# Optimization experiments

Hardware: AMD Instinct MI355X
Metric: run time of the kernel (lower is better)

## Reference

```python
import jax, jax.numpy as jnp
import numpy as np

B, S, D = 1, 2048, 4096          # batch, seqlen, model dim
H, KVH, HD = 32, 8, 128          # query heads, kv heads, head dim
W = 1024                         # sliding window
ROPE_THETA = 10000.0


def _rope(t, cos, sin):
    # t: [b, s, h, hd]; complex pairing matches torch.view_as_complex on reshape(..., hd//2, 2)
    a = t[..., 0::2]
    b = t[..., 1::2]
    out_r = a * cos - b * sin
    out_i = a * sin + b * cos
    return jnp.stack([out_r, out_i], axis=-1).reshape(t.shape)


def setup_inputs() -> dict:
    key = jax.random.key(0)
    ks = jax.random.split(key, 5)
    x = jax.random.normal(ks[0], (1, B, S, D), dtype=jnp.float32)
    wq = jax.random.normal(ks[1], (H * HD, D), dtype=jnp.float32) * 0.02
    wk = jax.random.normal(ks[2], (KVH * HD, D), dtype=jnp.float32) * 0.02
    wv = jax.random.normal(ks[3], (KVH * HD, D), dtype=jnp.float32) * 0.02
    wo = jax.random.normal(ks[4], (D, H * HD), dtype=jnp.float32) * 0.02
    # rotary frequencies: freqs_cis[s, hd/2] = exp(i * s * theta^{-2k/hd})
    inv_freq = 1.0 / (ROPE_THETA ** (jnp.arange(0, HD, 2, dtype=jnp.float32) / HD))
    angles = jnp.arange(S, dtype=jnp.float32)[:, None] * inv_freq[None, :]  # [S, HD/2]
    freqs_cos = jnp.cos(angles)
    freqs_sin = jnp.sin(angles)
    # sliding-window causal mask (additive)
    i = jnp.arange(S)
    allowed = (i[:, None] >= i[None, :]) & (i[:, None] - i[None, :] < W)
    mask = jnp.where(allowed, 0.0, -1e9).astype(jnp.float32)
    positions = jnp.arange(S, dtype=jnp.int64)
    return {"x": x, "wq": wq, "wk": wk, "wv": wv, "wo": wo,
            "freqs_cos": freqs_cos, "freqs_sin": freqs_sin,
            "mask": mask, "positions": positions}


def reference(x, wq, wk, wv, wo, freqs_cos, freqs_sin, mask, positions):
    xs = x[0]                                   # [B, S, D]
    xq = (xs @ wq.T).reshape(B, S, H, HD)
    xk = (xs @ wk.T).reshape(B, S, KVH, HD)
    xv = (xs @ wv.T).reshape(B, S, KVH, HD)
    cos = freqs_cos[None, :, None, :]           # [1, S, 1, HD/2]
    sin = freqs_sin[None, :, None, :]
    xq = _rope(xq, cos, sin)
    xk = _rope(xk, cos, sin)
    # GQA: repeat_interleave kv heads to match query heads (prefill path)
    rep = H // KVH
    k = jnp.repeat(xk, rep, axis=2)             # [B, S, H, HD]
    v = jnp.repeat(xv, rep, axis=2)
    scale = HD ** -0.5
    scores = jnp.einsum('bqhd,bkhd->bhqk', xq, k) * scale + mask[None, None]
    probs = jax.nn.softmax(scores, axis=-1)
    out = jnp.einsum('bhqk,bkhd->bqhd', probs, v).reshape(B, S, H * HD)
    return (out @ wo.T)[None]                   # [1, B, S, D]
```

## Files before the change

### kernel.cpp

```cpp
#include <hip/hip_runtime.h>
#include <hip/hip_bf16.h>


typedef __attribute__((ext_vector_type(8))) short short8;
typedef __attribute__((ext_vector_type(4))) float floatx4;
typedef unsigned short u16;
typedef unsigned int u32;

__device__ __forceinline__ u16 f2bf(float f) {
  u32 u = __builtin_bit_cast(u32, f);
  u32 r = u + 0x7FFFu + ((u >> 16) & 1u);
  return (u16)(r >> 16);
}

#define GLDS16(g, l)                                                     \
  __builtin_amdgcn_global_load_lds(                                      \
      (const __attribute__((address_space(1))) u32*)(g),                 \
      (__attribute__((address_space(3))) u32*)(l), 16, 0, 0)

#define SB() __builtin_amdgcn_sched_barrier(0)

__global__ __launch_bounds__(256) void cast_all(
    const float* __restrict__ x, const float* __restrict__ wq,
    const float* __restrict__ wk, const float* __restrict__ wv,
    const float* __restrict__ wo, u16* __restrict__ xb, u16* __restrict__ wqb,
    u16* __restrict__ wkb, u16* __restrict__ wvb, u16* __restrict__ wob) {
  const int tid = blockIdx.x * blockDim.x + threadIdx.x;
  const int stride = gridDim.x * blockDim.x;
  auto seg = [&](const float* __restrict__ in, u16* __restrict__ out, int n4) {
    for (int i = tid; i < n4; i += stride) {
      float4 v = ((const float4*)in)[i];
      ushort4 o;
      o.x = f2bf(v.x); o.y = f2bf(v.y); o.z = f2bf(v.z); o.w = f2bf(v.w);
      ((ushort4*)out)[i] = o;
    }
  };
  seg(x, xb, 2097152);
  seg(wq, wqb, 4194304);
  seg(wk, wkb, 1048576);
  seg(wv, wvb, 1048576);
  seg(wo, wob, 4194304);
}

template <int IS_QKV>
__global__ __launch_bounds__(512, 2) void gemm_t(
    const u16* __restrict__ A, const u16* __restrict__ B, void* __restrict__ Cq,
    u16* __restrict__ Ck, u16* __restrict__ Cv, const float* __restrict__ fcos,
    const float* __restrict__ fsin) {
  constexpr int BM = IS_QKV ? 256 : 128;
  constexpr int BN = IS_QKV ? 192 : 256;
  constexpr int MFR = BM / 32;
  constexpr int NFR = BN / 64;
  constexpr int WC = BN / 4;
  constexpr int ASZ = BM * 128;
  constexpr int BSZ = BN * 128;
  constexpr int NCA = ASZ / 8192;
  constexpr int NCB = BSZ / 8192;
  __shared__ u16 lds[(2 * ASZ + 3 * BSZ) / 2];
  const int K = 4096;

  int bm, bx;
  if constexpr (IS_QKV) {
    bm = blockIdx.x & 7;
    bx = blockIdx.x >> 3;
  } else {
    const int xcd = blockIdx.x & 7;
    const int j = blockIdx.x >> 3;
    bm = xcd * 2 + (j & 1);
    bx = j >> 1;
  }
  const int m0 = bm * BM, n0 = bx * BN;

  const int t = threadIdx.x, l = t & 63, w = t >> 6;
  const int li = l & 15, g = l >> 4;
  const int wm = w >> 2, wn = w & 3;

  const int srow = t >> 3;
  const int sslot = (t & 7) ^ (srow & 7);
  const u16* gA = A + (size_t)(m0 + srow) * K + sslot * 8;
  const u16* gB = B + (size_t)(n0 + srow) * K + sslot * 8;
  const int dst = t * 16;

  char* A0p = (char*)lds;
  char* A1p = A0p + ASZ;
  char* B0p = A0p + 2 * ASZ;
  char* B1p = B0p + BSZ;
  char* B2p = B1p + BSZ;

  auto stA = [&](char* base, int kt, int c) {
    GLDS16(gA + (size_t)c * 64 * K + kt, base + c * 8192 + dst);
  };
  auto stB = [&](char* base, int kt, int c) {
    GLDS16(gB + (size_t)c * 64 * K + kt, base + c * 8192 + dst);
  };

  int offA[2][MFR], offB[2][NFR];
#pragma unroll
  for (int kh = 0; kh < 2; kh++) {
#pragma unroll
    for (int mf = 0; mf < MFR; mf++) {
      int r = wm * (BM / 2) + mf * 16 + li;
      offA[kh][mf] = r * 128 + ((((kh << 2) | g) ^ (r & 7)) << 4);
    }
#pragma unroll
    for (int nf = 0; nf < NFR; nf++) {
      int r = wn * WC + nf * 16 + li;
      offB[kh][nf] = r * 128 + ((((kh << 2) | g) ^ (r & 7)) << 4);
    }
  }

  floatx4 acc[MFR][NFR] = {};
  const int NT = K / 64;

#pragma unroll
  for (int c = 0; c < NCB; c++) stB(B0p, 0, c);
#pragma unroll
  for (int c = 0; c < NCA; c++) stA(A0p, 0, c);
#pragma unroll
  for (int c = 0; c < NCB; c++) stB(B1p, 64, c);
  if constexpr (IS_QKV) asm volatile("s_waitcnt vmcnt(3)" ::: "memory");
  else                  asm volatile("s_waitcnt vmcnt(4)" ::: "memory");
  __builtin_amdgcn_s_barrier();

  for (int tt = 0; tt < NT; ++tt) {
    const char* Ac = A0p;
    const char* Bc = B0p;
    const int kt1 = (tt + 1) * 64, kt2 = (tt + 2) * 64;
    const bool s1 = (tt + 1 < NT), s2 = (tt + 2 < NT);

    if constexpr (IS_QKV) {
      short8 afr[4], bfr[NFR];
#pragma unroll
      for (int nf = 0; nf < NFR; nf++) bfr[nf] = *(const short8*)(Bc + offB[0][nf]);
#pragma unroll
      for (int mf = 0; mf < 4; mf++) afr[mf] = *(const short8*)(Ac + offA[0][mf]);
      if (s1) { stA(A1p, kt1, 0); stA(A1p, kt1, 1); }
      SB(); __builtin_amdgcn_s_barrier();
      asm volatile("s_waitcnt lgkmcnt(0)" ::: "memory");
      SB(); __builtin_amdgcn_s_setprio(1);
#pragma unroll
      for (int mf = 0; mf < 4; mf++)
#pragma unroll
        for (int nf = 0; nf < NFR; nf++)
          acc[mf][nf] = __builtin_amdgcn_mfma_f32_16x16x32_bf16(afr[mf], bfr[nf], acc[mf][nf], 0, 0, 0);
      __builtin_amdgcn_s_setprio(0); SB(); __builtin_amdgcn_s_barrier();
#pragma unroll
      for (int mf = 0; mf < 4; mf++) afr[mf] = *(const short8*)(Ac + offA[0][4 + mf]);
      if (s1) { stA(A1p, kt1, 2); stA(A1p, kt1, 3); }
      SB(); __builtin_amdgcn_s_barrier();
      asm volatile("s_waitcnt lgkmcnt(0)" ::: "memory");
      SB(); __builtin_amdgcn_s_setprio(1);
#pragma unroll
      for (int mf = 0; mf < 4; mf++)
#pragma unroll
        for (int nf = 0; nf < NFR; nf++)
          acc[4 + mf][nf] = __builtin_amdgcn_mfma_f32_16x16x32_bf16(afr[mf], bfr[nf], acc[4 + mf][nf], 0, 0, 0);
      __builtin_amdgcn_s_setprio(0); SB(); __builtin_amdgcn_s_barrier();
#pragma unroll
      for (int nf = 0; nf < NFR; nf++) bfr[nf] = *(const short8*)(Bc + offB[1][nf]);
#pragma unroll
      for (int mf = 0; mf < 4; mf++) afr[mf] = *(const short8*)(Ac + offA[1][mf]);
      if (s2) { stB(B2p, kt2, 0); stB(B2p, kt2, 1); }
      SB(); __builtin_amdgcn_s_barrier();
      asm volatile("s_waitcnt lgkmcnt(0)" ::: "memory");
      SB(); __builtin_amdgcn_s_setprio(1);
#pragma unroll
      for (int mf = 0; mf < 4; mf++)
#pragma unroll
        for (int nf = 0; nf < NFR; nf++)
          acc[mf][nf] = __builtin_amdgcn_mfma_f32_16x16x32_bf16(afr[mf], bfr[nf], acc[mf][nf], 0, 0, 0);
      __builtin_amdgcn_s_setprio(0); SB(); __builtin_amdgcn_s_barrier();
#pragma unroll
      for (int mf = 0; mf < 4; mf++) afr[mf] = *(const short8*)(Ac + offA[1][4 + mf]);
      if (s2) stB(B2p, kt2, 2);
      SB(); __builtin_amdgcn_s_barrier();
      asm volatile("s_waitcnt lgkmcnt(0)" ::: "memory");
      SB(); __builtin_amdgcn_s_setprio(1);
#pragma unroll
      for (int mf = 0; mf < 4; mf++)
#pragma unroll
        for (int nf = 0; nf < NFR; nf++)
          acc[4 + mf][nf] = __builtin_amdgcn_mfma_f32_16x16x32_bf16(afr[mf], bfr[nf], acc[4 + mf][nf], 0, 0, 0);
      __builtin_amdgcn_s_setprio(0);
      if (s2) asm volatile("s_waitcnt vmcnt(3)" ::: "memory");
      else    asm volatile("s_waitcnt vmcnt(0)" ::: "memory");
      SB(); __builtin_amdgcn_s_barrier();
    } else {
      short8 afr[4], bfr[2];
#pragma unroll
      for (int mf = 0; mf < 4; mf++) afr[mf] = *(const short8*)(Ac + offA[0][mf]);
#pragma unroll
      for (int nf = 0; nf < 2; nf++) bfr[nf] = *(const short8*)(Bc + offB[0][nf]);
      if (s1) { stA(A1p, kt1, 0); stA(A1p, kt1, 1); }
      SB(); __builtin_amdgcn_s_barrier();
      asm volatile("s_waitcnt lgkmcnt(0)" ::: "memory");
      SB(); __builtin_amdgcn_s_setprio(1);
#pragma unroll
      for (int mf = 0; mf < 4; mf++)
#pragma unroll
        for (int nf = 0; nf < 2; nf++)
          acc[mf][nf] = __builtin_amdgcn_mfma_f32_16x16x32_bf16(afr[mf], bfr[nf], acc[mf][nf], 0, 0, 0);
      __builtin_amdgcn_s_setprio(0); SB(); __builtin_amdgcn_s_barrier();
#pragma unroll
      for (int nf = 0; nf < 2; nf++) bfr[nf] = *(const short8*)(Bc + offB[0][2 + nf]);
      if (s2) { stB(B2p, kt2, 0); stB(B2p, kt2, 1); }
      SB(); __builtin_amdgcn_s_barrier();
      asm volatile("s_waitcnt lgkmcnt(0)" ::: "memory");
      SB(); __builtin_amdgcn_s_setprio(1);
#pragma unroll
      for (int mf = 0; mf < 4; mf++)
#pragma unroll
        for (int nf = 0; nf < 2; nf++)
          acc[mf][2 + nf] = __builtin_amdgcn_mfma_f32_16x16x32_bf16(afr[mf], bfr[nf], acc[mf][2 + nf], 0, 0, 0);
      __builtin_amdgcn_s_setprio(0); SB(); __builtin_amdgcn_s_barrier();
#pragma unroll
      for (int mf = 0; mf < 4; mf++) afr[mf] = *(const short8*)(Ac + offA[1][mf]);
#pragma unroll
      for (int nf = 0; nf < 2; nf++) bfr[nf] = *(const short8*)(Bc + offB[1][nf]);
      if (s2) stB(B2p, kt2, 2);
      SB(); __builtin_amdgcn_s_barrier();
      asm volatile("s_waitcnt lgkmcnt(0)" ::: "memory");
      SB(); __builtin_amdgcn_s_setprio(1);
#pragma unroll
      for (int mf = 0; mf < 4; mf++)
#pragma unroll
        for (int nf = 0; nf < 2; nf++)
          acc[mf][nf] = __builtin_amdgcn_mfma_f32_16x16x32_bf16(afr[mf], bfr[nf], acc[mf][nf], 0, 0, 0);
      __builtin_amdgcn_s_setprio(0); SB(); __builtin_amdgcn_s_barrier();
#pragma unroll
      for (int nf = 0; nf < 2; nf++) bfr[nf] = *(const short8*)(Bc + offB[1][2 + nf]);
      if (s2) stB(B2p, kt2, 3);
      SB(); __builtin_amdgcn_s_barrier();
      asm volatile("s_waitcnt lgkmcnt(0)" ::: "memory");
      SB(); __builtin_amdgcn_s_setprio(1);
#pragma unroll
      for (int mf = 0; mf < 4; mf++)
#pragma unroll
        for (int nf = 0; nf < 2; nf++)
          acc[mf][2 + nf] = __builtin_amdgcn_mfma_f32_16x16x32_bf16(afr[mf], bfr[nf], acc[mf][2 + nf], 0, 0, 0);
      __builtin_amdgcn_s_setprio(0);
      if (s2) asm volatile("s_waitcnt vmcnt(4)" ::: "memory");
      else    asm volatile("s_waitcnt vmcnt(0)" ::: "memory");
      SB(); __builtin_amdgcn_s_barrier();
    }

    char* tmpA = A0p; A0p = A1p; A1p = tmpA;
    char* tmpB = B0p; B0p = B1p; B1p = B2p; B2p = tmpB;
  }

  const float scale = 0.08838834764831845f;
#pragma unroll
  for (int mf = 0; mf < MFR; mf++) {
#pragma unroll
    for (int nf = 0; nf < NFR; nf++) {
      const int row0 = m0 + wm * (BM / 2) + mf * 16 + 4 * g;
      const int c = n0 + wn * WC + nf * 16 + li;
      if constexpr (!IS_QKV) {
        float* Cf = (float*)Cq;
#pragma unroll
        for (int r = 0; r < 4; r++) Cf[(size_t)(row0 + r) * 4096 + c] = acc[mf][nf][r];
      } else {
        if (c < 5120) {
          const int hd = c & 127;
          const int pp = hd >> 1;
          const bool even = (hd & 1) == 0;
#pragma unroll
          for (int r = 0; r < 4; r++) {
            const int row = row0 + r;
            float cv = fcos[row * 64 + pp];
            float sv = fsin[row * 64 + pp];
            float v = acc[mf][nf][r];
            float pv = __shfl_xor(v, 1);
            float o = even ? (v * cv - pv * sv) : (pv * sv + v * cv);
            if (c < 4096) {
              ((u16*)Cq)[(size_t)row * 4096 + c] = f2bf(o * scale);
            } else {
              Ck[(size_t)row * 1024 + (c - 4096)] = f2bf(o);
            }
          }
        } else {
          u32 lo = (u32)f2bf(acc[mf][nf][0]) | ((u32)f2bf(acc[mf][nf][1]) << 16);
          u32 hi = (u32)f2bf(acc[mf][nf][2]) | ((u32)f2bf(acc[mf][nf][3]) << 16);
          uint2 val; val.x = lo; val.y = hi;
          *(uint2*)(&Cv[(size_t)(c - 5120) * 2048 + row0]) = val;
        }
      }
    }
  }
}

__global__ __launch_bounds__(256) void attn_kernel(const u16* __restrict__ Q,
                                                   const u16* __restrict__ K,
                                                   const u16* __restrict__ Vt,
                                                   u16* __restrict__ O) {
  __shared__ u16 Ks[2][64 * 128];
  __shared__ u16 Vs[2][128 * 64];
  __shared__ u16 Ps[4][16 * 72];

  const int t = threadIdx.x, l = t & 63, w = t >> 6;
  const int li = l & 15, g = l >> 4;
  const int q0 = blockIdx.x * 64;
  const int h = blockIdx.y;
  const int kvh = h >> 2;
  const int qw = q0 + w * 16;

  short8 qf[4];
  {
    const u16* qp = Q + (size_t)(qw + li) * 4096 + h * 128 + g * 8;
#pragma unroll
    for (int kk = 0; kk < 4; kk++) qf[kk] = *(const short8*)(qp + kk * 32);
  }

  const u16* gK[4];
  const u16* gV[4];
  int ldsOff[4];
#pragma unroll
  for (int i = 0; i < 4; i++) {
    int rK = 16 * w + 4 * i + (l >> 4);
    int sK = (l & 15) ^ (rK & 7);
    gK[i] = K + (size_t)rK * 1024 + kvh * 128 + sK * 8;
    int rV = 32 * w + 8 * i + (l >> 3);
    int sV = (l & 7) ^ (rV & 7);
    gV[i] = Vt + (size_t)(kvh * 128 + rV) * 2048 + sV * 8;
    ldsOff[i] = (4 * w + i) * 1024;
  }

  int offK[4][4];
#pragma unroll
  for (int n = 0; n < 4; n++) {
    int r = 16 * n + li;
#pragma unroll
    for (int kk = 0; kk < 4; kk++)
      offK[n][kk] = r * 256 + (((kk * 4 + g) ^ (r & 7)) << 4);
  }
  int offV[2][8];
#pragma unroll
  for (int kb = 0; kb < 2; kb++)
#pragma unroll
    for (int dt = 0; dt < 8; dt++) {
      int d = dt * 16 + li;
      offV[kb][dt] = d * 128 + (((kb * 4 + g) ^ (d & 7)) << 4);
    }

  float mrow[4] = {-1e30f, -1e30f, -1e30f, -1e30f};
  float lsum[4] = {0.f, 0.f, 0.f, 0.f};
  floatx4 accO[8] = {};

  int klo = q0 - 1023;
  if (klo < 0) klo = 0;
  klo &= ~63;
  const int nt = (q0 + 64 - klo) >> 6;

  auto stage = [&](int buf, int k0) {
    char* ksb = (char*)&Ks[buf][0];
    char* vsb = (char*)&Vs[buf][0];
#pragma unroll
    for (int i = 0; i < 4; i++) GLDS16(gK[i] + (size_t)k0 * 1024, ksb + ldsOff[i]);
#pragma unroll
    for (int i = 0; i < 4; i++) GLDS16(gV[i] + k0, vsb + ldsOff[i]);
  };

  stage(0, klo);
  asm volatile("s_waitcnt vmcnt(0)" ::: "memory");
  __builtin_amdgcn_s_barrier();

  for (int it = 0; it < nt; it++) {
    const int k0 = klo + (it << 6);
    if (it + 1 < nt) stage((it + 1) & 1, k0 + 64);

    if (k0 <= qw + 15 && k0 + 63 >= qw - 1023) {
      const char* kb = (const char*)&Ks[it & 1][0];
      const char* vb = (const char*)&Vs[it & 1][0];
      floatx4 s[4] = {};
      __builtin_amdgcn_s_setprio(1);
#pragma unroll
      for (int kk = 0; kk < 4; kk++)
#pragma unroll
        for (int n = 0; n < 4; n++) {
          short8 kf = *(const short8*)(kb + offK[n][kk]);
          s[n] = __builtin_amdgcn_mfma_f32_16x16x32_bf16(qf[kk], kf, s[n], 0, 0, 0);
        }
      __builtin_amdgcn_s_setprio(0);
      const bool full = (k0 + 63 <= qw) && (k0 >= qw + 15 - 1023);
      if (!full) {
#pragma unroll
        for (int n = 0; n < 4; n++) {
          const int kc = k0 + n * 16 + li;
#pragma unroll
          for (int r = 0; r < 4; r++) {
            const int qr = qw + 4 * g + r;
            if (kc > qr || qr - kc > 1023) s[n][r] = -__builtin_inff();
          }
        }
      }
      float rm[4];
#pragma unroll
      for (int r = 0; r < 4; r++)
        rm[r] = fmaxf(fmaxf(s[0][r], s[1][r]), fmaxf(s[2][r], s[3][r]));
#pragma unroll
      for (int msk = 1; msk <= 8; msk <<= 1)
#pragma unroll
        for (int r = 0; r < 4; r++) rm[r] = fmaxf(rm[r], __shfl_xor(rm[r], msk));
      float al[4];
#pragma unroll
      for (int r = 0; r < 4; r++) {
        float mn = fmaxf(mrow[r], rm[r]);
        al[r] = __expf(mrow[r] - mn);
        mrow[r] = mn;
        lsum[r] *= al[r];
      }
#pragma unroll
      for (int dt = 0; dt < 8; dt++)
#pragma unroll
        for (int r = 0; r < 4; r++) accO[dt][r] *= al[r];
      float rs[4] = {0.f, 0.f, 0.f, 0.f};
      u16* pw = &Ps[w][0];
#pragma unroll
      for (int n = 0; n < 4; n++)
#pragma unroll
        for (int r = 0; r < 4; r++) {
          float p = __expf(s[n][r] - mrow[r]);
          rs[r] += p;
          pw[(4 * g + r) * 72 + n * 16 + li] = f2bf(p);
        }
#pragma unroll
      for (int msk = 1; msk <= 8; msk <<= 1)
#pragma unroll
        for (int r = 0; r < 4; r++) rs[r] += __shfl_xor(rs[r], msk);
#pragma unroll
      for (int r = 0; r < 4; r++) lsum[r] += rs[r];
      short8 pa[2];
#pragma unroll
      for (int kbi = 0; kbi < 2; kbi++)
        pa[kbi] = *(const short8*)((const char*)&Ps[w][0] + li * 144 + kbi * 64 + g * 16);
      __builtin_amdgcn_s_setprio(1);
#pragma unroll
      for (int kbi = 0; kbi < 2; kbi++)
#pragma unroll
        for (int dt = 0; dt < 8; dt++) {
          short8 vf = *(const short8*)(vb + offV[kbi][dt]);
          accO[dt] = __builtin_amdgcn_mfma_f32_16x16x32_bf16(pa[kbi], vf, accO[dt], 0, 0, 0);
        }
      __builtin_amdgcn_s_setprio(0);
    }
    asm volatile("s_waitcnt vmcnt(0)" ::: "memory");
    __builtin_amdgcn_s_barrier();
  }

  float inv[4];
#pragma unroll
  for (int r = 0; r < 4; r++) inv[r] = 1.0f / lsum[r];
#pragma unroll
  for (int dt = 0; dt < 8; dt++)
#pragma unroll
    for (int r = 0; r < 4; r++)
      O[(size_t)(qw + 4 * g + r) * 4096 + h * 128 + dt * 16 + li] =
          f2bf(accO[dt][r] * inv[r]);
}

extern "C" void kernel_launch(void* const* d_in, const int* in_sizes, int n_in,
                              void* d_out, int out_size, void* d_ws, size_t ws_size,
                              hipStream_t stream) {
  const float* x    = (const float*)d_in[0];
  const float* wq   = (const float*)d_in[1];
  const float* wk   = (const float*)d_in[2];
  const float* wv   = (const float*)d_in[3];
  const float* wo   = (const float*)d_in[4];
  const float* fcos = (const float*)d_in[5];
  const float* fsin = (const float*)d_in[6];

  u16* ws  = (u16*)d_ws;
  u16* xb  = ws;
  u16* wqb = xb + 8388608;
  u16* wkb = wqb + 16777216;
  u16* wvb = wkb + 4194304;
  u16* wob = wvb + 4194304;
  u16* Qb  = wob + 16777216;
  u16* Kb  = Qb + 8388608;
  u16* Vtb = Kb + 2097152;
  u16* AOb = Vtb + 2097152;

  cast_all<<<2048, 256, 0, stream>>>(x, wq, wk, wv, wo, xb, wqb, wkb, wvb, wob);
  gemm_t<1><<<256, 512, 0, stream>>>(xb, wqb, Qb, Kb, Vtb, fcos, fsin);
  attn_kernel<<<dim3(32, 32), 256, 0, stream>>>(Qb, Kb, Vtb, AOb);
  gemm_t<0><<<256, 512, 0, stream>>>(AOb, wob, d_out, nullptr, nullptr, nullptr, nullptr);
}
```

Baseline: 321.0 us.

## Collapse GEMM K-loop into two phases and drop intra-iteration barriers

Restructures the main GEMM loop for both QKV and output projections into two half-K phases per 64-wide tile. Each phase loads full A/B fragments for that phase, then issues all MFMAs, with a single barrier at the end of the iteration instead of a barrier, lgkmcnt wait and setprio around every quarter. The goal is to cut synchronization overhead and let the compiler interleave LDS reads with MFMAs. In exchange it raises register pressure from the larger fragment arrays and drops the explicit wave priority and LDS-wait scheduling. It also relies on the compiler to insert correct LDS waits.

```diff
diff --git a/kernel.cpp b/kernel.cpp
--- a/kernel.cpp
+++ b/kernel.cpp
@@ -123,125 +123,64 @@
   __builtin_amdgcn_s_barrier();
 
   for (int tt = 0; tt < NT; ++tt) {
+    SB();
     const char* Ac = A0p;
     const char* Bc = B0p;
     const int kt1 = (tt + 1) * 64, kt2 = (tt + 2) * 64;
     const bool s1 = (tt + 1 < NT), s2 = (tt + 2 < NT);
 
     if constexpr (IS_QKV) {
-      short8 afr[4], bfr[NFR];
-#pragma unroll
-      for (int nf = 0; nf < NFR; nf++) bfr[nf] = *(const short8*)(Bc + offB[0][nf]);
-#pragma unroll
-      for (int mf = 0; mf < 4; mf++) afr[mf] = *(const short8*)(Ac + offA[0][mf]);
-      if (s1) { stA(A1p, kt1, 0); stA(A1p, kt1, 1); }
-      SB(); __builtin_amdgcn_s_barrier();
-      asm volatile("s_waitcnt lgkmcnt(0)" ::: "memory");
-      SB(); __builtin_amdgcn_s_setprio(1);
-#pragma unroll
-      for (int mf = 0; mf < 4; mf++)
-#pragma unroll
-        for (int nf = 0; nf < NFR; nf++)
-          acc[mf][nf] = __builtin_amdgcn_mfma_f32_16x16x32_bf16(afr[mf], bfr[nf], acc[mf][nf], 0, 0, 0);
-      __builtin_amdgcn_s_setprio(0); SB(); __builtin_amdgcn_s_barrier();
-#pragma unroll
-      for (int mf = 0; mf < 4; mf++) afr[mf] = *(const short8*)(Ac + offA[0][4 + mf]);
-      if (s1) { stA(A1p, kt1, 2); stA(A1p, kt1, 3); }
-      SB(); __builtin_amdgcn_s_barrier();
-      asm volatile("s_waitcnt lgkmcnt(0)" ::: "memory");
-      SB(); __builtin_amdgcn_s_setprio(1);
-#pragma unroll
-      for (int mf = 0; mf < 4; mf++)
-#pragma unroll
-        for (int nf = 0; nf < NFR; nf++)
-          acc[4 + mf][nf] = __builtin_amdgcn_mfma_f32_16x16x32_bf16(afr[mf], bfr[nf], acc[4 + mf][nf], 0, 0, 0);
-      __builtin_amdgcn_s_setprio(0); SB(); __builtin_amdgcn_s_barrier();
-#pragma unroll
-      for (int nf = 0; nf < NFR; nf++) bfr[nf] = *(const short8*)(Bc + offB[1][nf]);
-#pragma unroll
-      for (int mf = 0; mf < 4; mf++) afr[mf] = *(const short8*)(Ac + offA[1][mf]);
-      if (s2) { stB(B2p, kt2, 0); stB(B2p, kt2, 1); }
-      SB(); __builtin_amdgcn_s_barrier();
-      asm volatile("s_waitcnt lgkmcnt(0)" ::: "memory");
-      SB(); __builtin_amdgcn_s_setprio(1);
-#pragma unroll
-      for (int mf = 0; mf < 4; mf++)
-#pragma unroll
-        for (int nf = 0; nf < NFR; nf++)
-          acc[mf][nf] = __builtin_amdgcn_mfma_f32_16x16x32_bf16(afr[mf], bfr[nf], acc[mf][nf], 0, 0, 0);
-      __builtin_amdgcn_s_setprio(0); SB(); __builtin_amdgcn_s_barrier();
-#pragma unroll
-      for (int mf = 0; mf < 4; mf++) afr[mf] = *(const short8*)(Ac + offA[1][4 + mf]);
-      if (s2) stB(B2p, kt2, 2);
-      SB(); __builtin_amdgcn_s_barrier();
-      asm volatile("s_waitcnt lgkmcnt(0)" ::: "memory");
-      SB(); __builtin_amdgcn_s_setprio(1);
-#pragma unroll
-      for (int mf = 0; mf < 4; mf++)
-#pragma unroll
-        for (int nf = 0; nf < NFR; nf++)
-          acc[4 + mf][nf] = __builtin_amdgcn_mfma_f32_16x16x32_bf16(afr[mf], bfr[nf], acc[4 + mf][nf], 0, 0, 0);
-      __builtin_amdgcn_s_setprio(0);
+      short8 a0[8], b0[3], a1[8], b1[3];
+#pragma unroll
+      for (int nf = 0; nf < 3; nf++) b0[nf] = *(const short8*)(Bc + offB[0][nf]);
+#pragma unroll
+      for (int mf = 0; mf < 8; mf++) a0[mf] = *(const short8*)(Ac + offA[0][mf]);
+      if (s1) { stA(A1p, kt1, 0); stA(A1p, kt1, 1); stA(A1p, kt1, 2); stA(A1p, kt1, 3); }
+#pragma unroll
+      for (int mf = 0; mf < 8; mf++)
+#pragma unroll
+        for (int nf = 0; nf < 3; nf++)
+          acc[mf][nf] = __builtin_amdgcn_mfma_f32_16x16x32_bf16(a0[mf], b0[nf], acc[mf][nf], 0, 0, 0);
+#pragma unroll
+      for (int nf = 0; nf < 3; nf++) b1[nf] = *(const short8*)(Bc + offB[1][nf]);
+#pragma unroll
+      for (int mf = 0; mf < 8; mf++) a1[mf] = *(const short8*)(Ac + offA[1][mf]);
+      if (s2) { stB(B2p, kt2, 0); stB(B2p, kt2, 1); stB(B2p, kt2, 2); }
+#pragma unroll
+      for (int mf = 0; mf < 8; mf++)
+#pragma unroll
+        for (int nf = 0; nf < 3; nf++)
+          acc[mf][nf] = __builtin_amdgcn_mfma_f32_16x16x32_bf16(a1[mf], b1[nf], acc[mf][nf], 0, 0, 0);
+      SB();
       if (s2) asm volatile("s_waitcnt vmcnt(3)" ::: "memory");
       else    asm volatile("s_waitcnt vmcnt(0)" ::: "memory");
-      SB(); __builtin_amdgcn_s_barrier();
+      __builtin_amdgcn_s_barrier();
     } else {
-      short8 afr[4], bfr[2];
-#pragma unroll
-      for (int mf = 0; mf < 4; mf++) afr[mf] = *(const short8*)(Ac + offA[0][mf]);
-#pragma unroll
-      for (int nf = 0; nf < 2; nf++) bfr[nf] = *(const short8*)(Bc + offB[0][nf]);
+      short8 a0[4], b0[4], a1[4], b1[4];
+#pragma unroll
+      for (int mf = 0; mf < 4; mf++) a0[mf] = *(const short8*)(Ac + offA[0][mf]);
+#pragma unroll
+      for (int nf = 0; nf < 4; nf++) b0[nf] = *(const short8*)(Bc + offB[0][nf]);
       if (s1) { stA(A1p, kt1, 0); stA(A1p, kt1, 1); }
-      SB(); __builtin_amdgcn_s_barrier();
-      asm volatile("s_waitcnt lgkmcnt(0)" ::: "memory");
-      SB(); __builtin_amdgcn_s_setprio(1);
 #pragma unroll
       for (int mf = 0; mf < 4; mf++)
 #pragma unroll
-        for (int nf = 0; nf < 2; nf++)
-          acc[mf][nf] = __builtin_amdgcn_mfma_f32_16x16x32_bf16(afr[mf], bfr[nf], acc[mf][nf], 0, 0, 0);
-      __builtin_amdgcn_s_setprio(0); SB(); __builtin_amdgcn_s_barrier();
-#pragma unroll
-      for (int nf = 0; nf < 2; nf++) bfr[nf] = *(const short8*)(Bc + offB[0][2 + nf]);
-      if (s2) { stB(B2p, kt2, 0); stB(B2p, kt2, 1); }
-      SB(); __builtin_amdgcn_s_barrier();
-      asm volatile("s_waitcnt lgkmcnt(0)" ::: "memory");
-      SB(); __builtin_amdgcn_s_setprio(1);
+        for (int nf = 0; nf < 4; nf++)
+          acc[mf][nf] = __builtin_amdgcn_mfma_f32_16x16x32_bf16(a0[mf], b0[nf], acc[mf][nf], 0, 0, 0);
+#pragma unroll
+      for (int mf = 0; mf < 4; mf++) a1[mf] = *(const short8*)(Ac + offA[1][mf]);
+#pragma unroll
+      for (int nf = 0; nf < 4; nf++) b1[nf] = *(const short8*)(Bc + offB[1][nf]);
+      if (s2) { stB(B2p, kt2, 0); stB(B2p, kt2, 1); stB(B2p, kt2, 2); stB(B2p, kt2, 3); }
 #pragma unroll
       for (int mf = 0; mf < 4; mf++)
 #pragma unroll
-        for (int nf = 0; nf < 2; nf++)
-          acc[mf][2 + nf] = __builtin_amdgcn_mfma_f32_16x16x32_bf16(afr[mf], bfr[nf], acc[mf][2 + nf], 0, 0, 0);
-      __builtin_amdgcn_s_setprio(0); SB(); __builtin_amdgcn_s_barrier();
-#pragma unroll
-      for (int mf = 0; mf < 4; mf++) afr[mf] = *(const short8*)(Ac + offA[1][mf]);
-#pragma unroll
-      for (int nf = 0; nf < 2; nf++) bfr[nf] = *(const short8*)(Bc + offB[1][nf]);
-      if (s2) stB(B2p, kt2, 2);
-      SB(); __builtin_amdgcn_s_barrier();
-      asm volatile("s_waitcnt lgkmcnt(0)" ::: "memory");
-      SB(); __builtin_amdgcn_s_setprio(1);
-#pragma unroll
-      for (int mf = 0; mf < 4; mf++)
-#pragma unroll
-        for (int nf = 0; nf < 2; nf++)
-          acc[mf][nf] = __builtin_amdgcn_mfma_f32_16x16x32_bf16(afr[mf], bfr[nf], acc[mf][nf], 0, 0, 0);
-      __builtin_amdgcn_s_setprio(0); SB(); __builtin_amdgcn_s_barrier();
-#pragma unroll
-      for (int nf = 0; nf < 2; nf++) bfr[nf] = *(const short8*)(Bc + offB[1][2 + nf]);
-      if (s2) stB(B2p, kt2, 3);
-      SB(); __builtin_amdgcn_s_barrier();
-      asm volatile("s_waitcnt lgkmcnt(0)" ::: "memory");
-      SB(); __builtin_amdgcn_s_setprio(1);
-#pragma unroll
-      for (int mf = 0; mf < 4; mf++)
-#pragma unroll
-        for (int nf = 0; nf < 2; nf++)
-          acc[mf][2 + nf] = __builtin_amdgcn_mfma_f32_16x16x32_bf16(afr[mf], bfr[nf], acc[mf][2 + nf], 0, 0, 0);
-      __builtin_amdgcn_s_setprio(0);
+        for (int nf = 0; nf < 4; nf++)
+          acc[mf][nf] = __builtin_amdgcn_mfma_f32_16x16x32_bf16(a1[mf], b1[nf], acc[mf][nf], 0, 0, 0);
+      SB();
       if (s2) asm volatile("s_waitcnt vmcnt(4)" ::: "memory");
       else    asm volatile("s_waitcnt vmcnt(0)" ::: "memory");
-      SB(); __builtin_amdgcn_s_barrier();
+      __builtin_amdgcn_s_barrier();
     }
 
     char* tmpA = A0p; A0p = A1p; A1p = tmpA;
```

Result: faster. 314.7 us (-2.0%).
